# Performance work log

Hardware: AMD Instinct MI355X
Metric: run time of the kernel (lower is better)

## Reference

```python
import jax, jax.numpy as jnp
import numpy as np

NUM_USERS = 100_000
NUM_JOBS = 100_000
N_NODES = NUM_USERS + NUM_JOBS
E = 3_200_000
D = 64  # embedding_dim == hidden_dim
B = 16_384


def setup_inputs() -> dict:
    key = jax.random.key(0)
    ks = jax.random.split(key, 10)
    edge_index = jax.random.randint(ks[0], (2, E), 0, N_NODES, dtype=jnp.int64)
    user_indices = jax.random.randint(ks[1], (B,), 0, NUM_USERS, dtype=jnp.int64)
    job_indices = jax.random.randint(ks[2], (B,), 0, NUM_JOBS, dtype=jnp.int64)
    # parameters (match reset_parameters: embeddings std=0.1, xavier pred, zero bias)
    user_emb_w = 0.1 * jax.random.normal(ks[3], (NUM_USERS, D), dtype=jnp.float32)
    job_emb_w = 0.1 * jax.random.normal(ks[4], (NUM_JOBS, D), dtype=jnp.float32)
    W1 = jax.random.normal(ks[5], (D, D), dtype=jnp.float32) / np.sqrt(D)
    b1 = jnp.zeros((D,), dtype=jnp.float32)
    W2 = jax.random.normal(ks[6], (D, D), dtype=jnp.float32) / np.sqrt(D)
    b2 = jnp.zeros((D,), dtype=jnp.float32)
    lim = np.sqrt(6.0 / (2 * D + 1))
    pred_w = jax.random.uniform(ks[7], (2 * D, 1), dtype=jnp.float32, minval=-lim, maxval=lim)
    pred_b = jnp.zeros((1,), dtype=jnp.float32)
    return {
        "edge_index": edge_index, "user_indices": user_indices, "job_indices": job_indices,
        "user_emb_w": user_emb_w, "job_emb_w": job_emb_w,
        "W1": W1, "b1": b1, "W2": W2, "b2": b2,
        "pred_w": pred_w, "pred_b": pred_b,
    }


def reference(edge_index, user_indices, job_indices, user_emb_w, job_emb_w, W1, b1, W2, b2, pred_w, pred_b):
    num_users = user_emb_w.shape[0]
    n = num_users + job_emb_w.shape[0]
    x = jnp.concatenate([user_emb_w, job_emb_w], axis=0)  # [N, D]

    # GCNConv (PyG defaults): add self-loops, symmetric D^-1/2 (A+I) D^-1/2 normalization
    loops = jnp.arange(n, dtype=edge_index.dtype)
    row = jnp.concatenate([edge_index[0], loops])  # source nodes
    col = jnp.concatenate([edge_index[1], loops])  # target nodes
    deg = jax.ops.segment_sum(jnp.ones_like(col, dtype=x.dtype), col, num_segments=n)
    dinv = jnp.where(deg > 0, jax.lax.rsqrt(jnp.maximum(deg, 1e-12)), 0.0)
    norm = dinv[row] * dinv[col]  # [E+N]

    def gcn_conv(h, W, b):
        h = h @ W                                   # [N, D]
        msg = h[row] * norm[:, None]                # gather + scale, [E+N, D]
        agg = jax.ops.segment_sum(msg, col, num_segments=n)  # scatter-add
        return agg + b

    x = jax.nn.relu(gcn_conv(x, W1, b1))  # dropout is identity at inference
    x = gcn_conv(x, W2, b2)

    user_emb = x[user_indices]                      # [B, D]
    job_emb = x[num_users + job_indices]            # [B, D]
    combined = jnp.concatenate([user_emb, job_emb], axis=1)  # [B, 2D]
    return (combined @ pred_w + pred_b)[:, 0]       # [B]
```

## Files before the change

kernel.cpp:

```cpp
#include <hip/hip_runtime.h>
#include <hip/hip_fp16.h>

#define D 64
#define BSHIFT 10
#define BMASK ((1 << BSHIFT) - 1)
#define NBUK_MAX 256
#define T_TILE 6144
#define EPT 24
#define CAP 20480

#if defined(__has_builtin)
#if __has_builtin(__builtin_amdgcn_fdot2)
#define HAVE_FDOT2 1
#endif
#endif

typedef _Float16 h2f __attribute__((ext_vector_type(2)));
typedef _Float16 half8v __attribute__((ext_vector_type(8)));
typedef float f4v __attribute__((ext_vector_type(4)));

__device__ __forceinline__ int wave_iscan(int v, int lane) {
#pragma unroll
    for (int off = 1; off < 64; off <<= 1) {
        int u = __shfl_up(v, off, 64);
        if (lane >= off) v += u;
    }
    return v;
}

__device__ __forceinline__ int block_escan(int v, int tid, int* wtot ) {
    int lane = tid & 63, w = tid >> 6;
    int inc = wave_iscan(v, lane);
    if (lane == 63) wtot[w] = inc;
    __syncthreads();
    int addv = 0;
#pragma unroll
    for (int q = 0; q < 4; q++) addv += (q < w) ? wtot[q] : 0;
    return inc - v + addv;
}

__device__ __forceinline__ float4 h4_to_f4(uint2 u) {
    __half2 a = *(__half2*)&u.x, b = *(__half2*)&u.y;
    float2 fa = __half22float2(a), fb = __half22float2(b);
    return make_float4(fa.x, fa.y, fb.x, fb.y);
}

__device__ __forceinline__ void acc_u2(float* acc, uint2 u) {
#ifdef HAVE_FDOT2
    h2f a0, a1;
    __builtin_memcpy(&a0, &u.x, 4);
    __builtin_memcpy(&a1, &u.y, 4);
    const h2f LO = {(_Float16)1.0f, (_Float16)0.0f};
    const h2f HI = {(_Float16)0.0f, (_Float16)1.0f};
    acc[0] = __builtin_amdgcn_fdot2(a0, LO, acc[0], false);
    acc[1] = __builtin_amdgcn_fdot2(a0, HI, acc[1], false);
    acc[2] = __builtin_amdgcn_fdot2(a1, LO, acc[2], false);
    acc[3] = __builtin_amdgcn_fdot2(a1, HI, acc[3], false);
#else
    float4 v = h4_to_f4(u);
    acc[0] += v.x; acc[1] += v.y; acc[2] += v.z; acc[3] += v.w;
#endif
}

__device__ __forceinline__ void acc_u4(float* acc, uint4 u) {
    uint2 a; a.x = u.x; a.y = u.y;
    uint2 b; b.x = u.z; b.y = u.w;
    acc_u2(acc, a);
    acc_u2(acc + 4, b);
}


__global__ __launch_bounds__(256) void k_bin(const int* __restrict__ row, const int* __restrict__ col,
                                             int E, int* __restrict__ bbase,
                                             unsigned* __restrict__ ebuf, int nbuk,
                                             const float* __restrict__ W1, const float* __restrict__ W2,
                                             __half* __restrict__ WT1, __half* __restrict__ WT2) {
    __shared__ int hist4[4][NBUK_MAX];
    __shared__ int sexcl[NBUK_MAX];
    __shared__ int cur4[4][NBUK_MAX];
    __shared__ int gbase[NBUK_MAX];
    __shared__ int wtot[4];
    __shared__ unsigned stage[T_TILE];
    __shared__ unsigned char sbuk[T_TILE];
    int tid = threadIdx.x;
    int w = tid >> 6;
    int tile0 = blockIdx.x * T_TILE;
    int cnt = min(T_TILE, E - tile0);

    if (blockIdx.x < 2) {
        const float* Ws = blockIdx.x ? W2 : W1;
        __half* Wd = blockIdx.x ? WT2 : WT1;
#pragma unroll
        for (int i = 0; i < 16; i++) {
            int f = i * 256 + tid;
            int k = f >> 6, c = f & 63;
            Wd[c * 64 + k] = __float2half(Ws[f]);
        }
    }

    unsigned pk[EPT];
    int bk[EPT];

#pragma unroll
    for (int q = 0; q < 4; q++) hist4[q][tid] = 0;
    __syncthreads();
#pragma unroll
    for (int j = 0; j < EPT; j++) {
        int i = tid + j * 256;
        if (i < cnt) {
            int r = row[tile0 + i];
            int c = col[tile0 + i];
            bk[j] = c >> BSHIFT;
            pk[j] = ((unsigned)(c & BMASK) << 18) | (unsigned)r;
            atomicAdd(&hist4[w][bk[j]], 1);
        } else {
            bk[j] = -1;
        }
    }
    __syncthreads();

    int h0 = hist4[0][tid], h1 = hist4[1][tid], h2 = hist4[2][tid], h3 = hist4[3][tid];
    int v = h0 + h1 + h2 + h3;
    int excl = block_escan(v, tid, wtot);
    sexcl[tid] = excl;
    cur4[0][tid] = excl;
    cur4[1][tid] = excl + h0;
    cur4[2][tid] = excl + h0 + h1;
    cur4[3][tid] = excl + h0 + h1 + h2;
    gbase[tid] = (v > 0 && tid < nbuk) ? (tid * CAP + atomicAdd(&bbase[tid], v)) : 0;
    __syncthreads();

#pragma unroll
    for (int j = 0; j < EPT; j++) {
        if (bk[j] >= 0) {
            int p = atomicAdd(&cur4[w][bk[j]], 1);
            stage[p] = pk[j];
            sbuk[p] = (unsigned char)bk[j];
        }
    }
    __syncthreads();

    for (int i = tid; i < cnt; i += 256) {
        int b = sbuk[i];
        int gpos = gbase[b] + (i - sexcl[b]);
        ebuf[gpos] = stage[i];
    }
}


__global__ __launch_bounds__(256) void k_csr2a(const unsigned* __restrict__ ebuf,
                                               const int* __restrict__ bbase, int N,
                                               int2* __restrict__ rps, float* __restrict__ dinv,
                                               __half* __restrict__ h) {
    __shared__ int lcnt[1 << BSHIFT];
    __shared__ int wtot[4];
    int tid = threadIdx.x;
    int c0 = blockIdx.x << BSHIFT;
    int nn = min(1 << BSHIFT, N - c0);
    int e0 = blockIdx.x * CAP, e1 = e0 + bbase[blockIdx.x];

    if (blockIdx.x == 0 && tid < 16) {
        uint2 z; z.x = 0u; z.y = 0u;
        *(uint2*)(h + (size_t)N * D + tid * 4) = z;
    }

    for (int i = tid; i < (1 << BSHIFT); i += 256) lcnt[i] = 0;
    __syncthreads();
    for (int j = e0 + tid; j < e1; j += 256)
        atomicAdd(&lcnt[ebuf[j] >> 18], 1);
    __syncthreads();

    int c[4]; int s = 0;
#pragma unroll
    for (int i = 0; i < 4; i++) { c[i] = lcnt[tid * 4 + i]; s += c[i]; }
    int run = block_escan(s, tid, wtot);
#pragma unroll
    for (int i = 0; i < 4; i++) {
        int idx = tid * 4 + i;
        if (idx < nn) {
            int st = e0 + run;
            rps[c0 + idx] = make_int2(st, st + c[i]);
            dinv[c0 + idx] = rsqrtf((float)(c[i] + 1));
        }
        run += c[i];
    }
}


__device__ __forceinline__ void stage_Wt(const __half* __restrict__ WTg, __half* __restrict__ Wt, int tid) {
#pragma unroll
    for (int i = 0; i < 2; i++) {
        int f = (i * 256 + tid) * 8;
        int c = f >> 6, k = f & 63;
        *(half8v*)(Wt + c * 72 + k) = *(const half8v*)(WTg + f);
    }
}

__device__ __forceinline__ void gemm_compute(const __half* __restrict__ Xh, const __half* __restrict__ Wt,
                                             int n0, int N, const float* __restrict__ dinvp,
                                             __half* __restrict__ out, int tid) {
    int lane = tid & 63;
    int wv = tid >> 6;
    int n16 = lane & 15, quad = lane >> 4;
    const __half* Xw = Xh + (wv * 16) * 72;
    half8v a0 = *(const half8v*)(Xw + n16 * 72 + quad * 8);
    half8v a1 = *(const half8v*)(Xw + n16 * 72 + quad * 8 + 32);
    f4v acc[4];
#pragma unroll
    for (int ct = 0; ct < 4; ct++) {
        acc[ct] = (f4v){0.f, 0.f, 0.f, 0.f};
        const __half* wp = Wt + (ct * 16 + n16) * 72;
        half8v b0 = *(const half8v*)(wp + quad * 8);
        half8v b1 = *(const half8v*)(wp + quad * 8 + 32);
        acc[ct] = __builtin_amdgcn_mfma_f32_16x16x32_f16(a0, b0, acc[ct], 0, 0, 0);
        acc[ct] = __builtin_amdgcn_mfma_f32_16x16x32_f16(a1, b1, acc[ct], 0, 0, 0);
    }
#pragma unroll
    for (int r = 0; r < 4; r++) {
        int node = n0 + wv * 16 + quad * 4 + r;
        if (node < N) {
            float dv = dinvp[node];
#pragma unroll
            for (int ct = 0; ct < 4; ct++)
                out[(size_t)node * D + ct * 16 + n16] = __float2half(acc[ct][r] * dv);
        }
    }
}


__global__ __launch_bounds__(256) void k_csr2b_gemm1(const unsigned* __restrict__ ebuf,
                                                     const int2* __restrict__ rps,
                                                     const int* __restrict__ bbase,
                                                     int N, int nbuk, int* __restrict__ srcs,
                                                     const float* __restrict__ xu, const float* __restrict__ xj,
                                                     int U, const __half* __restrict__ WT1,
                                                     const float* __restrict__ dinv, __half* __restrict__ h) {
    __shared__ __align__(16) __half Xh[64 * 72];
    __shared__ __align__(16) __half Wt[64 * 72];
    int tid = threadIdx.x;
    if ((int)blockIdx.x < nbuk) {
        int* lcur = (int*)Xh;
        int c0 = blockIdx.x << BSHIFT;
        int e0 = blockIdx.x * CAP, e1 = e0 + bbase[blockIdx.x];
        for (int i = tid; i < (1 << BSHIFT); i += 256)
            lcur[i] = (c0 + i < N) ? rps[c0 + i].x : 0;
        __syncthreads();
        for (int j = e0 + tid; j < e1; j += 256) {
            unsigned pk = ebuf[j];
            int p = atomicAdd(&lcur[pk >> 18], 1);
            srcs[p] = (int)(pk & 0x3ffffu);
        }
    } else {
        int n0 = ((int)blockIdx.x - nbuk) * 64;
        stage_Wt(WT1, Wt, tid);
#pragma unroll
        for (int i = 0; i < 4; i++) {
            int e4 = i * 256 + tid;
            int nl = e4 >> 4, k4 = e4 & 15;
            int nn = n0 + nl;
            uint2 st; st.x = 0u; st.y = 0u;
            if (nn < N) {
                const float* src = (nn < U) ? (xu + (size_t)nn * D) : (xj + (size_t)(nn - U) * D);
                float4 v = *(const float4*)(src + k4 * 4);
                __half2 p0 = __floats2half2_rn(v.x, v.y);
                __half2 p1 = __floats2half2_rn(v.z, v.w);
                st.x = *(unsigned*)&p0; st.y = *(unsigned*)&p1;
            }
            *(uint2*)(Xh + nl * 72 + k4 * 4) = st;
        }
        __syncthreads();
        gemm_compute(Xh, Wt, n0, N, dinv, h, tid);
    }
}


__device__ __forceinline__ void gather8(float* acc, const __half* __restrict__ hs,
                                        const int2* __restrict__ rps,
                                        const int* __restrict__ srcs,
                                        int node, int N, int g, int t) {
    const __half* hp = hs + t * 8;
    int2 r = rps[node];
    int e0 = r.x, deg = r.y - r.x;
    for (int cb = 0; cb < deg; cb += 8) {
        int sv = (cb + t < deg) ? srcs[e0 + cb + t] : N;
        int base = g * 8;
        int s0 = __shfl(sv, base + 0, 64);
        int s1 = __shfl(sv, base + 1, 64);
        int s2 = __shfl(sv, base + 2, 64);
        int s3 = __shfl(sv, base + 3, 64);
        int s4 = __shfl(sv, base + 4, 64);
        int s5 = __shfl(sv, base + 5, 64);
        int s6 = __shfl(sv, base + 6, 64);
        int s7 = __shfl(sv, base + 7, 64);
        uint4 u0 = *(const uint4*)(hp + (size_t)s0 * D);
        uint4 u1 = *(const uint4*)(hp + (size_t)s1 * D);
        uint4 u2 = *(const uint4*)(hp + (size_t)s2 * D);
        uint4 u3 = *(const uint4*)(hp + (size_t)s3 * D);
        uint4 u4 = *(const uint4*)(hp + (size_t)s4 * D);
        uint4 u5 = *(const uint4*)(hp + (size_t)s5 * D);
        uint4 u6 = *(const uint4*)(hp + (size_t)s6 * D);
        uint4 u7 = *(const uint4*)(hp + (size_t)s7 * D);
        acc_u4(acc, u0);
        acc_u4(acc, u1);
        acc_u4(acc, u2);
        acc_u4(acc, u3);
        acc_u4(acc, u4);
        acc_u4(acc, u5);
        acc_u4(acc, u6);
        acc_u4(acc, u7);
    }
}


__global__ __launch_bounds__(256) void k_agg_gemm2(const __half* __restrict__ hs, const float* __restrict__ dinv,
                                                   const int2* __restrict__ rps, const int* __restrict__ srcs,
                                                   const float* __restrict__ bias, const __half* __restrict__ WT2,
                                                   const float* __restrict__ pw, int N,
                                                   float* __restrict__ zu, float* __restrict__ zj) {
    __shared__ __align__(16) __half Xh[64 * 72];
    __shared__ __align__(16) __half Wt[64 * 72];
    int tid = threadIdx.x;
    int lane = tid & 63;
    int w = tid >> 6;
    int g = lane >> 3, t = lane & 7;
    int n0 = blockIdx.x * 64;

    stage_Wt(WT2, Wt, tid);

    float4 ba = *(const float4*)(bias + t * 8);
    float4 bb = *(const float4*)(bias + t * 8 + 4);
#pragma unroll
    for (int rr = 0; rr < 2; rr++) {
        int nl = w * 16 + rr * 8 + g;
        int node = n0 + nl;
        uint4 st; st.x = 0u; st.y = 0u; st.z = 0u; st.w = 0u;
        if (node < N) {
            float acc[8] = {0.f, 0.f, 0.f, 0.f, 0.f, 0.f, 0.f, 0.f};
            gather8(acc, hs, rps, srcs, node, N, g, t);
            uint4 su = *(const uint4*)(hs + (size_t)node * D + t * 8);
            float4 sa = h4_to_f4(make_uint2(su.x, su.y));
            float4 sb = h4_to_f4(make_uint2(su.z, su.w));
            float dv = dinv[node];
            float o0 = fmaxf((acc[0] + sa.x) * dv + ba.x, 0.f);
            float o1 = fmaxf((acc[1] + sa.y) * dv + ba.y, 0.f);
            float o2 = fmaxf((acc[2] + sa.z) * dv + ba.z, 0.f);
            float o3 = fmaxf((acc[3] + sa.w) * dv + ba.w, 0.f);
            float o4 = fmaxf((acc[4] + sb.x) * dv + bb.x, 0.f);
            float o5 = fmaxf((acc[5] + sb.y) * dv + bb.y, 0.f);
            float o6 = fmaxf((acc[6] + sb.z) * dv + bb.z, 0.f);
            float o7 = fmaxf((acc[7] + sb.w) * dv + bb.w, 0.f);
            __half2 p0 = __floats2half2_rn(o0, o1);
            __half2 p1 = __floats2half2_rn(o2, o3);
            __half2 p2 = __floats2half2_rn(o4, o5);
            __half2 p3 = __floats2half2_rn(o6, o7);
            st.x = *(unsigned*)&p0; st.y = *(unsigned*)&p1;
            st.z = *(unsigned*)&p2; st.w = *(unsigned*)&p3;
        }
        *(uint4*)(Xh + nl * 72 + t * 8) = st;
    }
    __syncthreads();

    int wv = w;
    int n16 = lane & 15, quad = lane >> 4;
    const __half* Xw = Xh + (wv * 16) * 72;
    half8v a0 = *(const half8v*)(Xw + n16 * 72 + quad * 8);
    half8v a1 = *(const half8v*)(Xw + n16 * 72 + quad * 8 + 32);
    f4v acc[4];
    float pwu_r[4], pwj_r[4];
#pragma unroll
    for (int ct = 0; ct < 4; ct++) {
        pwu_r[ct] = pw[ct * 16 + n16];
        pwj_r[ct] = pw[64 + ct * 16 + n16];
        acc[ct] = (f4v){0.f, 0.f, 0.f, 0.f};
        const __half* wp = Wt + (ct * 16 + n16) * 72;
        half8v b0 = *(const half8v*)(wp + quad * 8);
        half8v b1 = *(const half8v*)(wp + quad * 8 + 32);
        acc[ct] = __builtin_amdgcn_mfma_f32_16x16x32_f16(a0, b0, acc[ct], 0, 0, 0);
        acc[ct] = __builtin_amdgcn_mfma_f32_16x16x32_f16(a1, b1, acc[ct], 0, 0, 0);
    }
#pragma unroll
    for (int r = 0; r < 4; r++) {
        int node = n0 + wv * 16 + quad * 4 + r;
        float dv = (node < N) ? dinv[node] : 0.0f;
        float su = acc[0][r] * pwu_r[0] + acc[1][r] * pwu_r[1]
                 + acc[2][r] * pwu_r[2] + acc[3][r] * pwu_r[3];
        float sj = acc[0][r] * pwj_r[0] + acc[1][r] * pwj_r[1]
                 + acc[2][r] * pwj_r[2] + acc[3][r] * pwj_r[3];
        su += __shfl_xor(su, 1, 64); sj += __shfl_xor(sj, 1, 64);
        su += __shfl_xor(su, 2, 64); sj += __shfl_xor(sj, 2, 64);
        su += __shfl_xor(su, 4, 64); sj += __shfl_xor(sj, 4, 64);
        su += __shfl_xor(su, 8, 64); sj += __shfl_xor(sj, 8, 64);
        if (n16 == 0 && node < N) {
            zu[node] = su * dv;
            zj[node] = sj * dv;
        }
    }
}


__global__ __launch_bounds__(256) void k_pred(const float* __restrict__ zu, const float* __restrict__ zj,
                                              const float* __restrict__ dinv,
                                              const int2* __restrict__ rps, const int* __restrict__ srcs,
                                              const float* __restrict__ b2, const float* __restrict__ pw,
                                              const float* __restrict__ pb,
                                              const int* __restrict__ uidx, const int* __restrict__ jidx,
                                              int U, int N, int B, float* __restrict__ out) {
    int tid = threadIdx.x;
    int lane = tid & 63;
    int g = lane >> 3, t = lane & 7;
    int pair = blockIdx.x * 16 + (tid >> 6) * 4 + (g >> 1);
    if (pair >= B) return;
    int side = g & 1;
    int c = side ? (U + jidx[pair]) : uidx[pair];
    const float* zt = side ? zj : zu;

    float4 b2a = *(const float4*)(b2 + t * 8);
    float4 b2b = *(const float4*)(b2 + t * 8 + 4);
    float4 wa = *(const float4*)(pw + side * 64 + t * 8);
    float4 wb = *(const float4*)(pw + side * 64 + t * 8 + 4);
    float cpart = b2a.x * wa.x + b2a.y * wa.y + b2a.z * wa.z + b2a.w * wa.w
                + b2b.x * wb.x + b2b.y * wb.y + b2b.z * wb.z + b2b.w * wb.w;

    int2 r = rps[c];
    int deg = r.y - r.x;
    float s = 0.f;
    for (int cb = 0; cb < deg; cb += 8) {
        if (cb + t < deg) s += zt[srcs[r.x + cb + t]];
    }
    s += __shfl_xor(s, 1, 64); cpart += __shfl_xor(cpart, 1, 64);
    s += __shfl_xor(s, 2, 64); cpart += __shfl_xor(cpart, 2, 64);
    s += __shfl_xor(s, 4, 64); cpart += __shfl_xor(cpart, 4, 64);

    float val = (s + zt[c]) * dinv[c] + cpart;
    val += __shfl_xor(val, 8, 64);
    if ((lane & 15) == 0) out[pair] = val + pb[0];
}


extern "C" void kernel_launch(void* const* d_in, const int* in_sizes, int n_in,
                              void* d_out, int out_size, void* d_ws, size_t ws_size,
                              hipStream_t stream) {
    const int*   edge = (const int*)d_in[0];
    const int*   uidx = (const int*)d_in[1];
    const int*   jidx = (const int*)d_in[2];
    const float* xu   = (const float*)d_in[3];
    const float* xj   = (const float*)d_in[4];
    const float* W1   = (const float*)d_in[5];
    const float* b1   = (const float*)d_in[6];
    const float* W2   = (const float*)d_in[7];
    const float* b2   = (const float*)d_in[8];
    const float* pw   = (const float*)d_in[9];
    const float* pb   = (const float*)d_in[10];
    float* out = (float*)d_out;

    int E = in_sizes[0] / 2;
    int B = in_sizes[1];
    int U = in_sizes[3] / D;
    int J = in_sizes[4] / D;
    int N = U + J;
    int nbuk = (N + (1 << BSHIFT) - 1) >> BSHIFT;
    const int* row = edge;
    const int* col = edge + E;

    char* p = (char*)d_ws;
    auto alloc = [&](size_t bytes) -> void* {
        void* q = (void*)p;
        p += (bytes + 255) / 256 * 256;
        return q;
    };
    size_t capsz = (size_t)nbuk * CAP * 4;
    int*      bbase = (int*)alloc(256 * 4);
    int2*     rps   = (int2*)alloc((size_t)N * 8);
    float*    dinv  = (float*)alloc((size_t)N * 4);
    int*      srcs  = (int*)alloc(capsz);
    __half*   h     = (__half*)alloc((size_t)(N + 1) * D * 2);
    unsigned* ebuf  = (unsigned*)alloc(capsz);
    float*    zu    = (float*)alloc((size_t)N * 4);
    float*    zj    = (float*)alloc((size_t)N * 4);
    __half*   WT1   = (__half*)alloc((size_t)D * D * 2);
    __half*   WT2   = (__half*)alloc((size_t)D * D * 2);

    hipMemsetAsync(bbase, 0, 256 * 4, stream);

    k_bin<<<(E + T_TILE - 1) / T_TILE, 256, 0, stream>>>(row, col, E, bbase, ebuf, nbuk,
                                                         W1, W2, WT1, WT2);

    k_csr2a<<<nbuk, 256, 0, stream>>>(ebuf, bbase, N, rps, dinv, h);

    k_csr2b_gemm1<<<nbuk + (N + 63) / 64, 256, 0, stream>>>(ebuf, rps, bbase, N, nbuk, srcs,
                                                            xu, xj, U, WT1, dinv, h);

    k_agg_gemm2<<<(N + 63) / 64, 256, 0, stream>>>(h, dinv, rps, srcs, b1, WT2, pw, N, zu, zj);

    k_pred<<<(B + 15) / 16, 256, 0, stream>>>(zu, zj, dinv, rps, srcs, b2, pw, pb,
                                              uidx, jidx, U, N, B, out);
}
```

Baseline: 259.0 us.

## Fuse edge binning with first GEMM and merge CSR passes into one kernel

The first X·W1 GEMM no longer needs the degree normalization, so it moves into the binning kernel as extra blocks that run alongside edge bucketing and write unscaled h. The two CSR kernels (count/scan and scatter of sources) merge into one kernel, which also rescales h rows by dinv in place. This cuts a kernel launch and overlaps the GEMM with binning. In exchange h makes an extra read-modify-write pass in half precision, and the binning blocks share a manually carved shared-memory buffer with the GEMM blocks.

```diff
diff --git a/kernel.cpp b/kernel.cpp
--- a/kernel.cpp
+++ b/kernel.cpp
@@ -8,6 +8,7 @@
 #define T_TILE 6144
 #define EPT 24
 #define CAP 20480
+#define SM_BYTES 40976
 
 #if defined(__has_builtin)
 #if __has_builtin(__builtin_amdgcn_fdot2)
@@ -70,189 +71,96 @@
 }
 
 
-__global__ __launch_bounds__(256) void k_bin(const int* __restrict__ row, const int* __restrict__ col,
-                                             int E, int* __restrict__ bbase,
-                                             unsigned* __restrict__ ebuf, int nbuk,
-                                             const float* __restrict__ W1, const float* __restrict__ W2,
-                                             __half* __restrict__ WT1, __half* __restrict__ WT2) {
-    __shared__ int hist4[4][NBUK_MAX];
-    __shared__ int sexcl[NBUK_MAX];
-    __shared__ int cur4[4][NBUK_MAX];
-    __shared__ int gbase[NBUK_MAX];
-    __shared__ int wtot[4];
-    __shared__ unsigned stage[T_TILE];
-    __shared__ unsigned char sbuk[T_TILE];
+__global__ __launch_bounds__(256) void k_bin_gemm1(const int* __restrict__ row, const int* __restrict__ col,
+                                                   int E, int nbin, int* __restrict__ bbase,
+                                                   unsigned* __restrict__ ebuf, int nbuk,
+                                                   const float* __restrict__ xu, const float* __restrict__ xj,
+                                                   int U, int N,
+                                                   const float* __restrict__ W1, const float* __restrict__ W2,
+                                                   __half* __restrict__ WT2, __half* __restrict__ h) {
+    __shared__ __align__(16) char smem[SM_BYTES];
     int tid = threadIdx.x;
-    int w = tid >> 6;
-    int tile0 = blockIdx.x * T_TILE;
-    int cnt = min(T_TILE, E - tile0);
-
-    if (blockIdx.x < 2) {
-        const float* Ws = blockIdx.x ? W2 : W1;
-        __half* Wd = blockIdx.x ? WT2 : WT1;
+
+    if ((int)blockIdx.x < nbin) {
+        int* hist4 = (int*)smem;
+        int* sexcl = (int*)(smem + 4096);
+        int* cur4  = (int*)(smem + 5120);
+        int* gbase = (int*)(smem + 9216);
+        int* wtot  = (int*)(smem + 10240);
+        unsigned* stage = (unsigned*)(smem + 10256);
+        unsigned char* sbuk = (unsigned char*)(smem + 34832);
+        int w = tid >> 6;
+        int tile0 = blockIdx.x * T_TILE;
+        int cnt = min(T_TILE, E - tile0);
+
+        unsigned pk[EPT];
+        int bk[EPT];
+
+#pragma unroll
+        for (int q = 0; q < 4; q++) hist4[q * NBUK_MAX + tid] = 0;
+        __syncthreads();
+#pragma unroll
+        for (int j = 0; j < EPT; j++) {
+            int i = tid + j * 256;
+            if (i < cnt) {
+                int r = row[tile0 + i];
+                int c = col[tile0 + i];
+                bk[j] = c >> BSHIFT;
+                pk[j] = ((unsigned)(c & BMASK) << 18) | (unsigned)r;
+                atomicAdd(&hist4[w * NBUK_MAX + bk[j]], 1);
+            } else {
+                bk[j] = -1;
+            }
+        }
+        __syncthreads();
+
+        int h0 = hist4[0 * NBUK_MAX + tid], h1 = hist4[1 * NBUK_MAX + tid];
+        int h2 = hist4[2 * NBUK_MAX + tid], h3 = hist4[3 * NBUK_MAX + tid];
+        int v = h0 + h1 + h2 + h3;
+        int excl = block_escan(v, tid, wtot);
+        sexcl[tid] = excl;
+        cur4[0 * NBUK_MAX + tid] = excl;
+        cur4[1 * NBUK_MAX + tid] = excl + h0;
+        cur4[2 * NBUK_MAX + tid] = excl + h0 + h1;
+        cur4[3 * NBUK_MAX + tid] = excl + h0 + h1 + h2;
+        gbase[tid] = (v > 0 && tid < nbuk) ? (tid * CAP + atomicAdd(&bbase[tid], v)) : 0;
+        __syncthreads();
+
+#pragma unroll
+        for (int j = 0; j < EPT; j++) {
+            if (bk[j] >= 0) {
+                int p = atomicAdd(&cur4[w * NBUK_MAX + bk[j]], 1);
+                stage[p] = pk[j];
+                sbuk[p] = (unsigned char)bk[j];
+            }
+        }
+        __syncthreads();
+
+        for (int i = tid; i < cnt; i += 256) {
+            int b = sbuk[i];
+            int gpos = gbase[b] + (i - sexcl[b]);
+            ebuf[gpos] = stage[i];
+        }
+    } else {
+        __half* Xh = (__half*)smem;
+        __half* Wt = (__half*)(smem + 9216);
+        int n0 = ((int)blockIdx.x - nbin) * 64;
+
+        if ((int)blockIdx.x == nbin) {
+#pragma unroll
+            for (int i = 0; i < 16; i++) {
+                int f = i * 256 + tid;
+                int k = f >> 6, c = f & 63;
+                WT2[c * 64 + k] = __float2half(W2[f]);
+            }
+        }
+
 #pragma unroll
         for (int i = 0; i < 16; i++) {
             int f = i * 256 + tid;
             int k = f >> 6, c = f & 63;
-            Wd[c * 64 + k] = __float2half(Ws[f]);
-        }
-    }
-
-    unsigned pk[EPT];
-    int bk[EPT];
-
-#pragma unroll
-    for (int q = 0; q < 4; q++) hist4[q][tid] = 0;
-    __syncthreads();
-#pragma unroll
-    for (int j = 0; j < EPT; j++) {
-        int i = tid + j * 256;
-        if (i < cnt) {
-            int r = row[tile0 + i];
-            int c = col[tile0 + i];
-            bk[j] = c >> BSHIFT;
-            pk[j] = ((unsigned)(c & BMASK) << 18) | (unsigned)r;
-            atomicAdd(&hist4[w][bk[j]], 1);
-        } else {
-            bk[j] = -1;
-        }
-    }
-    __syncthreads();
-
-    int h0 = hist4[0][tid], h1 = hist4[1][tid], h2 = hist4[2][tid], h3 = hist4[3][tid];
-    int v = h0 + h1 + h2 + h3;
-    int excl = block_escan(v, tid, wtot);
-    sexcl[tid] = excl;
-    cur4[0][tid] = excl;
-    cur4[1][tid] = excl + h0;
-    cur4[2][tid] = excl + h0 + h1;
-    cur4[3][tid] = excl + h0 + h1 + h2;
-    gbase[tid] = (v > 0 && tid < nbuk) ? (tid * CAP + atomicAdd(&bbase[tid], v)) : 0;
-    __syncthreads();
-
-#pragma unroll
-    for (int j = 0; j < EPT; j++) {
-        if (bk[j] >= 0) {
-            int p = atomicAdd(&cur4[w][bk[j]], 1);
-            stage[p] = pk[j];
-            sbuk[p] = (unsigned char)bk[j];
-        }
-    }
-    __syncthreads();
-
-    for (int i = tid; i < cnt; i += 256) {
-        int b = sbuk[i];
-        int gpos = gbase[b] + (i - sexcl[b]);
-        ebuf[gpos] = stage[i];
-    }
-}
-
-
-__global__ __launch_bounds__(256) void k_csr2a(const unsigned* __restrict__ ebuf,
-                                               const int* __restrict__ bbase, int N,
-                                               int2* __restrict__ rps, float* __restrict__ dinv,
-                                               __half* __restrict__ h) {
-    __shared__ int lcnt[1 << BSHIFT];
-    __shared__ int wtot[4];
-    int tid = threadIdx.x;
-    int c0 = blockIdx.x << BSHIFT;
-    int nn = min(1 << BSHIFT, N - c0);
-    int e0 = blockIdx.x * CAP, e1 = e0 + bbase[blockIdx.x];
-
-    if (blockIdx.x == 0 && tid < 16) {
-        uint2 z; z.x = 0u; z.y = 0u;
-        *(uint2*)(h + (size_t)N * D + tid * 4) = z;
-    }
-
-    for (int i = tid; i < (1 << BSHIFT); i += 256) lcnt[i] = 0;
-    __syncthreads();
-    for (int j = e0 + tid; j < e1; j += 256)
-        atomicAdd(&lcnt[ebuf[j] >> 18], 1);
-    __syncthreads();
-
-    int c[4]; int s = 0;
-#pragma unroll
-    for (int i = 0; i < 4; i++) { c[i] = lcnt[tid * 4 + i]; s += c[i]; }
-    int run = block_escan(s, tid, wtot);
-#pragma unroll
-    for (int i = 0; i < 4; i++) {
-        int idx = tid * 4 + i;
-        if (idx < nn) {
-            int st = e0 + run;
-            rps[c0 + idx] = make_int2(st, st + c[i]);
-            dinv[c0 + idx] = rsqrtf((float)(c[i] + 1));
-        }
-        run += c[i];
-    }
-}
-
-
-__device__ __forceinline__ void stage_Wt(const __half* __restrict__ WTg, __half* __restrict__ Wt, int tid) {
-#pragma unroll
-    for (int i = 0; i < 2; i++) {
-        int f = (i * 256 + tid) * 8;
-        int c = f >> 6, k = f & 63;
-        *(half8v*)(Wt + c * 72 + k) = *(const half8v*)(WTg + f);
-    }
-}
-
-__device__ __forceinline__ void gemm_compute(const __half* __restrict__ Xh, const __half* __restrict__ Wt,
-                                             int n0, int N, const float* __restrict__ dinvp,
-                                             __half* __restrict__ out, int tid) {
-    int lane = tid & 63;
-    int wv = tid >> 6;
-    int n16 = lane & 15, quad = lane >> 4;
-    const __half* Xw = Xh + (wv * 16) * 72;
-    half8v a0 = *(const half8v*)(Xw + n16 * 72 + quad * 8);
-    half8v a1 = *(const half8v*)(Xw + n16 * 72 + quad * 8 + 32);
-    f4v acc[4];
-#pragma unroll
-    for (int ct = 0; ct < 4; ct++) {
-        acc[ct] = (f4v){0.f, 0.f, 0.f, 0.f};
-        const __half* wp = Wt + (ct * 16 + n16) * 72;
-        half8v b0 = *(const half8v*)(wp + quad * 8);
-        half8v b1 = *(const half8v*)(wp + quad * 8 + 32);
-        acc[ct] = __builtin_amdgcn_mfma_f32_16x16x32_f16(a0, b0, acc[ct], 0, 0, 0);
-        acc[ct] = __builtin_amdgcn_mfma_f32_16x16x32_f16(a1, b1, acc[ct], 0, 0, 0);
-    }
-#pragma unroll
-    for (int r = 0; r < 4; r++) {
-        int node = n0 + wv * 16 + quad * 4 + r;
-        if (node < N) {
-            float dv = dinvp[node];
-#pragma unroll
-            for (int ct = 0; ct < 4; ct++)
-                out[(size_t)node * D + ct * 16 + n16] = __float2half(acc[ct][r] * dv);
-        }
-    }
-}
-
-
-__global__ __launch_bounds__(256) void k_csr2b_gemm1(const unsigned* __restrict__ ebuf,
-                                                     const int2* __restrict__ rps,
-                                                     const int* __restrict__ bbase,
-                                                     int N, int nbuk, int* __restrict__ srcs,
-                                                     const float* __restrict__ xu, const float* __restrict__ xj,
-                                                     int U, const __half* __restrict__ WT1,
-                                                     const float* __restrict__ dinv, __half* __restrict__ h) {
-    __shared__ __align__(16) __half Xh[64 * 72];
-    __shared__ __align__(16) __half Wt[64 * 72];
-    int tid = threadIdx.x;
-    if ((int)blockIdx.x < nbuk) {
-        int* lcur = (int*)Xh;
-        int c0 = blockIdx.x << BSHIFT;
-        int e0 = blockIdx.x * CAP, e1 = e0 + bbase[blockIdx.x];
-        for (int i = tid; i < (1 << BSHIFT); i += 256)
-            lcur[i] = (c0 + i < N) ? rps[c0 + i].x : 0;
-        __syncthreads();
-        for (int j = e0 + tid; j < e1; j += 256) {
-            unsigned pk = ebuf[j];
-            int p = atomicAdd(&lcur[pk >> 18], 1);
-            srcs[p] = (int)(pk & 0x3ffffu);
-        }
-    } else {
-        int n0 = ((int)blockIdx.x - nbuk) * 64;
-        stage_Wt(WT1, Wt, tid);
+            Wt[c * 72 + k] = __float2half(W1[f]);
+        }
 #pragma unroll
         for (int i = 0; i < 4; i++) {
             int e4 = i * 256 + tid;
@@ -269,7 +177,96 @@
             *(uint2*)(Xh + nl * 72 + k4 * 4) = st;
         }
         __syncthreads();
-        gemm_compute(Xh, Wt, n0, N, dinv, h, tid);
+
+        int lane = tid & 63;
+        int wv = tid >> 6;
+        int n16 = lane & 15, quad = lane >> 4;
+        const __half* Xw = Xh + (wv * 16) * 72;
+        half8v a0 = *(const half8v*)(Xw + n16 * 72 + quad * 8);
+        half8v a1 = *(const half8v*)(Xw + n16 * 72 + quad * 8 + 32);
+        f4v acc[4];
+#pragma unroll
+        for (int ct = 0; ct < 4; ct++) {
+            acc[ct] = (f4v){0.f, 0.f, 0.f, 0.f};
+            const __half* wp = Wt + (ct * 16 + n16) * 72;
+            half8v b0 = *(const half8v*)(wp + quad * 8);
+            half8v b1 = *(const half8v*)(wp + quad * 8 + 32);
+            acc[ct] = __builtin_amdgcn_mfma_f32_16x16x32_f16(a0, b0, acc[ct], 0, 0, 0);
+            acc[ct] = __builtin_amdgcn_mfma_f32_16x16x32_f16(a1, b1, acc[ct], 0, 0, 0);
+        }
+#pragma unroll
+        for (int r = 0; r < 4; r++) {
+            int node = n0 + wv * 16 + quad * 4 + r;
+            if (node < N) {
+#pragma unroll
+                for (int ct = 0; ct < 4; ct++)
+                    h[(size_t)node * D + ct * 16 + n16] = __float2half(acc[ct][r]);
+            }
+        }
+    }
+}
+
+
+__global__ __launch_bounds__(256) void k_csr(const unsigned* __restrict__ ebuf,
+                                             const int* __restrict__ bbase, int N,
+                                             int2* __restrict__ rps, float* __restrict__ dinv,
+                                             int* __restrict__ srcs, __half* __restrict__ h) {
+    __shared__ int lcnt[1 << BSHIFT];
+    __shared__ float ldinv[1 << BSHIFT];
+    __shared__ int wtot[4];
+    int tid = threadIdx.x;
+    int c0 = blockIdx.x << BSHIFT;
+    int nn = min(1 << BSHIFT, N - c0);
+    int e0 = blockIdx.x * CAP, e1 = e0 + bbase[blockIdx.x];
+
+    if (blockIdx.x == 0 && tid < 16) {
+        uint2 z; z.x = 0u; z.y = 0u;
+        *(uint2*)(h + (size_t)N * D + tid * 4) = z;
+    }
+
+    for (int i = tid; i < (1 << BSHIFT); i += 256) lcnt[i] = 0;
+    __syncthreads();
+    for (int j = e0 + tid; j < e1; j += 256)
+        atomicAdd(&lcnt[ebuf[j] >> 18], 1);
+    __syncthreads();
+
+    int c[4]; int s = 0;
+#pragma unroll
+    for (int i = 0; i < 4; i++) { c[i] = lcnt[tid * 4 + i]; s += c[i]; }
+    int run = block_escan(s, tid, wtot);
+#pragma unroll
+    for (int i = 0; i < 4; i++) {
+        int idx = tid * 4 + i;
+        int st = e0 + run;
+        float dv = rsqrtf((float)(c[i] + 1));
+        if (idx < nn) {
+            rps[c0 + idx] = make_int2(st, st + c[i]);
+            dinv[c0 + idx] = dv;
+        }
+        ldinv[idx] = (idx < nn) ? dv : 0.0f;
+        lcnt[idx] = st;
+        run += c[i];
+    }
+    __syncthreads();
+
+    for (int j = e0 + tid; j < e1; j += 256) {
+        unsigned pk = ebuf[j];
+        int p = atomicAdd(&lcnt[pk >> 18], 1);
+        srcs[p] = (int)(pk & 0x3ffffu);
+    }
+
+    for (int u = tid; u < nn * 8; u += 256) {
+        int i = u >> 3, q = u & 7;
+        float dv = ldinv[i];
+        __half* hp = h + ((size_t)(c0 + i) << 6) + q * 8;
+        uint4 x = *(uint4*)hp;
+        __half2* xp = (__half2*)&x;
+#pragma unroll
+        for (int m = 0; m < 4; m++) {
+            float2 f = __half22float2(xp[m]);
+            xp[m] = __floats2half2_rn(f.x * dv, f.y * dv);
+        }
+        *(uint4*)hp = x;
     }
 }
 
@@ -311,6 +308,15 @@
     }
 }
 
+__device__ __forceinline__ void stage_Wt(const __half* __restrict__ WTg, __half* __restrict__ Wt, int tid) {
+#pragma unroll
+    for (int i = 0; i < 2; i++) {
+        int f = (i * 256 + tid) * 8;
+        int c = f >> 6, k = f & 63;
+        *(half8v*)(Wt + c * 72 + k) = *(const half8v*)(WTg + f);
+    }
+}
+
 
 __global__ __launch_bounds__(256) void k_agg_gemm2(const __half* __restrict__ hs, const float* __restrict__ dinv,
                                                    const int2* __restrict__ rps, const int* __restrict__ srcs,
@@ -459,6 +465,8 @@
     int J = in_sizes[4] / D;
     int N = U + J;
     int nbuk = (N + (1 << BSHIFT) - 1) >> BSHIFT;
+    int nbin = (E + T_TILE - 1) / T_TILE;
+    int ngemm = (N + 63) / 64;
     const int* row = edge;
     const int* col = edge + E;
 
@@ -477,20 +485,16 @@
     unsigned* ebuf  = (unsigned*)alloc(capsz);
     float*    zu    = (float*)alloc((size_t)N * 4);
     float*    zj    = (float*)alloc((size_t)N * 4);
-    __half*   WT1   = (__half*)alloc((size_t)D * D * 2);
     __half*   WT2   = (__half*)alloc((size_t)D * D * 2);
 
     hipMemsetAsync(bbase, 0, 256 * 4, stream);
 
-    k_bin<<<(E + T_TILE - 1) / T_TILE, 256, 0, stream>>>(row, col, E, bbase, ebuf, nbuk,
-                                                         W1, W2, WT1, WT2);
-
-    k_csr2a<<<nbuk, 256, 0, stream>>>(ebuf, bbase, N, rps, dinv, h);
-
-    k_csr2b_gemm1<<<nbuk + (N + 63) / 64, 256, 0, stream>>>(ebuf, rps, bbase, N, nbuk, srcs,
-                                                            xu, xj, U, WT1, dinv, h);
-
-    k_agg_gemm2<<<(N + 63) / 64, 256, 0, stream>>>(h, dinv, rps, srcs, b1, WT2, pw, N, zu, zj);
+    k_bin_gemm1<<<nbin + ngemm, 256, 0, stream>>>(row, col, E, nbin, bbase, ebuf, nbuk,
+                                                  xu, xj, U, N, W1, W2, WT2, h);
+
+    k_csr<<<nbuk, 256, 0, stream>>>(ebuf, bbase, N, rps, dinv, srcs, h);
+
+    k_agg_gemm2<<<ngemm, 256, 0, stream>>>(h, dinv, rps, srcs, b1, WT2, pw, N, zu, zj);
 
     k_pred<<<(B + 15) / 16, 256, 0, stream>>>(zu, zj, dinv, rps, srcs, b2, pw, pb,
                                               uidx, jidx, U, N, B, out);
```

Result: slower. 271.1 us (+4.7%).
